# Performance work log

Measured on AMD Instinct MI355X. Metric: run time of the kernel, lower is better.

## Reference

```python
import jax, jax.numpy as jnp
import numpy as np

NEG = -jnp.finfo(jnp.float32).max


def setup_inputs() -> dict:
    key = jax.random.key(0)
    ks = jax.random.split(key, 5)
    B, N, C = 8, 1024, 768
    x = jax.random.normal(ks[0], (B, N, C), dtype=jnp.float32)
    qkv_w = jax.random.normal(ks[1], (3 * C, C), dtype=jnp.float32) * (C ** -0.5)
    qkv_b = jax.random.normal(ks[2], (3 * C,), dtype=jnp.float32) * 0.02
    proj_w = jax.random.normal(ks[3], (C, C), dtype=jnp.float32) * (C ** -0.5)
    proj_b = jax.random.normal(ks[4], (C,), dtype=jnp.float32) * 0.02
    return {"x": x, "qkv_w": qkv_w, "qkv_b": qkv_b, "proj_w": proj_w, "proj_b": proj_b, "k": 64}


def reference(x, qkv_w, qkv_b, proj_w, proj_b, k):
    B, N, C = x.shape
    H = 12
    d = C // H
    scale = d ** -0.5
    # qkv projection: [B,N,3C] -> [3,B,H,N,d]
    qkv = (x @ qkv_w.T + qkv_b).reshape(B, N, 3, H, d).transpose(2, 0, 3, 1, 4)
    q, kk, v = qkv[0], qkv[1], qkv[2]
    attn = jnp.einsum("bhqd,bhkd->bhqk", q, kk) * scale  # [B,H,N,N]
    if k > 0:
        top, _ = jax.lax.top_k(attn, k)
        vk = top[..., -1:]  # k-th largest per query row
        attn = jnp.where(attn < vk, NEG, attn)
    attn = jax.nn.softmax(attn, axis=-1)
    out = jnp.einsum("bhqk,bhkd->bhqd", attn, v)  # [B,H,N,d]
    out = out.transpose(0, 2, 1, 3).reshape(B, N, C)
    return out @ proj_w.T + proj_b
```

## Files before the change

kernel.cpp:

```cpp
#include <hip/hip_runtime.h>

constexpr int Bn = 8, Nn = 1024, Cn = 768, Hn = 12, Dn = 64;

typedef _Float16 f16x4 __attribute__((ext_vector_type(4)));
typedef _Float16 f16x8 __attribute__((ext_vector_type(8)));
typedef float    f32x4v __attribute__((ext_vector_type(4)));

__device__ __forceinline__ unsigned toOrd(float f) {
  unsigned u = __float_as_uint(f);
  return (u & 0x80000000u) ? ~u : (u | 0x80000000u);
}
__device__ __forceinline__ float invOrd(unsigned v) {
  unsigned b = (v & 0x80000000u) ? (v & 0x7FFFFFFFu) : ~v;
  return __uint_as_float(b);
}
__device__ __forceinline__ int lane_excl_cnt(unsigned long long m) {
  return __builtin_amdgcn_mbcnt_hi((unsigned)(m >> 32),
         __builtin_amdgcn_mbcnt_lo((unsigned)m, 0));
}

__device__ __forceinline__ float wave_sum_f32(float x) {
  int xi = __float_as_int(x);
  x += __int_as_float(__builtin_amdgcn_update_dpp(0, xi, 0x111, 0xF, 0xF, false)); xi = __float_as_int(x);
  x += __int_as_float(__builtin_amdgcn_update_dpp(0, xi, 0x112, 0xF, 0xF, false)); xi = __float_as_int(x);
  x += __int_as_float(__builtin_amdgcn_update_dpp(0, xi, 0x114, 0xF, 0xF, false)); xi = __float_as_int(x);
  x += __int_as_float(__builtin_amdgcn_update_dpp(0, xi, 0x118, 0xF, 0xF, false)); xi = __float_as_int(x);
  x += __int_as_float(__builtin_amdgcn_update_dpp(0, xi, 0x142, 0xA, 0xF, false)); xi = __float_as_int(x);
  x += __int_as_float(__builtin_amdgcn_update_dpp(0, xi, 0x143, 0xC, 0xF, false));
  return __int_as_float(__builtin_amdgcn_readlane(__float_as_int(x), 63));
}
__device__ __forceinline__ unsigned wave_max_u32(unsigned x) {
  int xi = (int)x;
  x = max(x, (unsigned)__builtin_amdgcn_update_dpp(xi, xi, 0x111, 0xF, 0xF, false)); xi = (int)x;
  x = max(x, (unsigned)__builtin_amdgcn_update_dpp(xi, xi, 0x112, 0xF, 0xF, false)); xi = (int)x;
  x = max(x, (unsigned)__builtin_amdgcn_update_dpp(xi, xi, 0x114, 0xF, 0xF, false)); xi = (int)x;
  x = max(x, (unsigned)__builtin_amdgcn_update_dpp(xi, xi, 0x118, 0xF, 0xF, false)); xi = (int)x;
  x = max(x, (unsigned)__builtin_amdgcn_update_dpp(xi, xi, 0x142, 0xA, 0xF, false)); xi = (int)x;
  x = max(x, (unsigned)__builtin_amdgcn_update_dpp(xi, xi, 0x143, 0xC, 0xF, false));
  return (unsigned)__builtin_amdgcn_readlane((int)x, 63);
}
__device__ __forceinline__ unsigned wave_min_u32(unsigned x) {
  int xi = (int)x;
  x = min(x, (unsigned)__builtin_amdgcn_update_dpp(xi, xi, 0x111, 0xF, 0xF, false)); xi = (int)x;
  x = min(x, (unsigned)__builtin_amdgcn_update_dpp(xi, xi, 0x112, 0xF, 0xF, false)); xi = (int)x;
  x = min(x, (unsigned)__builtin_amdgcn_update_dpp(xi, xi, 0x114, 0xF, 0xF, false)); xi = (int)x;
  x = min(x, (unsigned)__builtin_amdgcn_update_dpp(xi, xi, 0x118, 0xF, 0xF, false)); xi = (int)x;
  x = min(x, (unsigned)__builtin_amdgcn_update_dpp(xi, xi, 0x142, 0xA, 0xF, false)); xi = (int)x;
  x = min(x, (unsigned)__builtin_amdgcn_update_dpp(xi, xi, 0x143, 0xC, 0xF, false));
  return (unsigned)__builtin_amdgcn_readlane((int)x, 63);
}

__global__ __launch_bounds__(256) void qkv_gemm_mfma(
    const float* __restrict__ X, const float* __restrict__ W,
    const float* __restrict__ bias,
    _Float16* __restrict__ qhp, _Float16* __restrict__ qlp,
    _Float16* __restrict__ khp, _Float16* __restrict__ klp,
    float* __restrict__ vb)
{
  constexpr int LDH = 40;
  __shared__ _Float16 AhH[128*LDH];
  __shared__ _Float16 AhL[128*LDH];
  __shared__ _Float16 BhH[64*LDH];
  __shared__ _Float16 BhL[64*LDH];
  int t = threadIdx.x;
  int wv = t >> 6, lane = t & 63;
  int quad = lane >> 4, l16 = lane & 15;
  int mt = blockIdx.x & 63, nt = blockIdx.x >> 6;
  int m0 = mt*128, n0 = nt*64;
  const bool needLo = (n0 < 1536);
  const float* Ap = X + (size_t)m0*768;
  const float* Bp = W + (size_t)n0*768;
  f32x4v acc1[2][4] = {};
  f32x4v acc2[2][4] = {};
  for (int k0 = 0; k0 < 768; k0 += 32) {
    float4 av[4]; float4 bv[2];
#pragma unroll
    for (int i = 0; i < 4; ++i) {
      int q = t + i*256;
      av[i] = *(const float4*)(Ap + (size_t)(q>>3)*768 + k0 + (q&7)*4);
    }
#pragma unroll
    for (int i = 0; i < 2; ++i) {
      int q = t + i*256;
      bv[i] = *(const float4*)(Bp + (size_t)(q>>3)*768 + k0 + (q&7)*4);
    }
    __syncthreads();
#pragma unroll
    for (int i = 0; i < 4; ++i) {
      int q = t + i*256;
      f16x4 h;
      h[0]=(_Float16)av[i].x; h[1]=(_Float16)av[i].y;
      h[2]=(_Float16)av[i].z; h[3]=(_Float16)av[i].w;
      *(f16x4*)(&AhH[(q>>3)*LDH + (q&7)*4]) = h;
      if (needLo) {
        f16x4 l;
        l[0]=(_Float16)((av[i].x-(float)h[0])*2048.0f);
        l[1]=(_Float16)((av[i].y-(float)h[1])*2048.0f);
        l[2]=(_Float16)((av[i].z-(float)h[2])*2048.0f);
        l[3]=(_Float16)((av[i].w-(float)h[3])*2048.0f);
        *(f16x4*)(&AhL[(q>>3)*LDH + (q&7)*4]) = l;
      }
    }
#pragma unroll
    for (int i = 0; i < 2; ++i) {
      int q = t + i*256;
      f16x4 h;
      h[0]=(_Float16)bv[i].x; h[1]=(_Float16)bv[i].y;
      h[2]=(_Float16)bv[i].z; h[3]=(_Float16)bv[i].w;
      *(f16x4*)(&BhH[(q>>3)*LDH + (q&7)*4]) = h;
      if (needLo) {
        f16x4 l;
        l[0]=(_Float16)((bv[i].x-(float)h[0])*2048.0f);
        l[1]=(_Float16)((bv[i].y-(float)h[1])*2048.0f);
        l[2]=(_Float16)((bv[i].z-(float)h[2])*2048.0f);
        l[3]=(_Float16)((bv[i].w-(float)h[3])*2048.0f);
        *(f16x4*)(&BhL[(q>>3)*LDH + (q&7)*4]) = l;
      }
    }
    __syncthreads();
    if (needLo) {
      f16x8 bfh[4], bfl[4];
#pragma unroll
      for (int ni = 0; ni < 4; ++ni) {
        bfh[ni] = *(f16x8*)(&BhH[(ni*16+l16)*LDH + quad*8]);
        bfl[ni] = *(f16x8*)(&BhL[(ni*16+l16)*LDH + quad*8]);
      }
#pragma unroll
      for (int mi = 0; mi < 2; ++mi) {
        f16x8 afh = *(f16x8*)(&AhH[(wv*32+mi*16+l16)*LDH + quad*8]);
        f16x8 afl = *(f16x8*)(&AhL[(wv*32+mi*16+l16)*LDH + quad*8]);
#pragma unroll
        for (int ni = 0; ni < 4; ++ni) {
          acc1[mi][ni] = __builtin_amdgcn_mfma_f32_16x16x32_f16(afh, bfh[ni], acc1[mi][ni], 0, 0, 0);
          acc2[mi][ni] = __builtin_amdgcn_mfma_f32_16x16x32_f16(afh, bfl[ni], acc2[mi][ni], 0, 0, 0);
          acc2[mi][ni] = __builtin_amdgcn_mfma_f32_16x16x32_f16(afl, bfh[ni], acc2[mi][ni], 0, 0, 0);
        }
      }
    } else {
      f16x8 bfh[4];
#pragma unroll
      for (int ni = 0; ni < 4; ++ni)
        bfh[ni] = *(f16x8*)(&BhH[(ni*16+l16)*LDH + quad*8]);
#pragma unroll
      for (int mi = 0; mi < 2; ++mi) {
        f16x8 afh = *(f16x8*)(&AhH[(wv*32+mi*16+l16)*LDH + quad*8]);
#pragma unroll
        for (int ni = 0; ni < 4; ++ni)
          acc1[mi][ni] = __builtin_amdgcn_mfma_f32_16x16x32_f16(afh, bfh[ni], acc1[mi][ni], 0, 0, 0);
      }
    }
  }
  int which = n0 / Cn;
  int rem0 = n0 - which*Cn;
  int h0 = rem0 >> 6;
  float sc = which == 0 ? 0.125f : 1.0f;
#pragma unroll
  for (int ni = 0; ni < 4; ++ni) {
    float bsv = bias[n0 + ni*16 + l16];
    int dd = (ni*16 + l16) & 63;
#pragma unroll
    for (int mi = 0; mi < 2; ++mi)
#pragma unroll
      for (int r = 0; r < 4; ++r) {
        int gm = m0 + wv*32 + mi*16 + quad*4 + r;
        int bbi = gm >> 10, nn = gm & 1023;
        size_t idx = (((size_t)(bbi*Hn + h0))*Nn + nn)*Dn + dd;
        float val = (acc1[mi][ni][r] + acc2[mi][ni][r] * (1.0f/2048.0f) + bsv) * sc;
        if (which == 2) {
          vb[idx] = val;
        } else {
          _Float16 hh = (_Float16)val;
          _Float16 ll = (_Float16)((val - (float)hh) * 2048.0f);
          if (which == 0) { qhp[idx] = hh; qlp[idx] = ll; }
          else            { khp[idx] = hh; klp[idx] = ll; }
        }
      }
  }
}

template <typename Epi>
__device__ __forceinline__ void mfma_gemm_body(
    const float* __restrict__ Xp, const float* __restrict__ Wp, Epi epi)
{
  constexpr int LDH = 40;
  __shared__ _Float16 Ah[128*LDH];
  __shared__ _Float16 Bh[64*LDH];
  int t = threadIdx.x;
  int wv = t >> 6, lane = t & 63;
  int quad = lane >> 4, l16 = lane & 15;
  int mt = blockIdx.x & 63, nt = blockIdx.x >> 6;
  int m0 = mt*128, n0 = nt*64;
  f32x4v acc[2][4] = {};
  for (int k0 = 0; k0 < 768; k0 += 32) {
    float4 av[4]; float4 bv[2];
#pragma unroll
    for (int i = 0; i < 4; ++i) {
      int q = t + i*256;
      av[i] = *(const float4*)(Xp + (size_t)(m0+(q>>3))*768 + k0 + (q&7)*4);
    }
#pragma unroll
    for (int i = 0; i < 2; ++i) {
      int q = t + i*256;
      bv[i] = *(const float4*)(Wp + (size_t)(n0+(q>>3))*768 + k0 + (q&7)*4);
    }
    __syncthreads();
#pragma unroll
    for (int i = 0; i < 4; ++i) {
      int q = t + i*256;
      f16x4 h; h[0]=(_Float16)av[i].x; h[1]=(_Float16)av[i].y;
               h[2]=(_Float16)av[i].z; h[3]=(_Float16)av[i].w;
      *(f16x4*)(&Ah[(q>>3)*LDH + (q&7)*4]) = h;
    }
#pragma unroll
    for (int i = 0; i < 2; ++i) {
      int q = t + i*256;
      f16x4 h; h[0]=(_Float16)bv[i].x; h[1]=(_Float16)bv[i].y;
               h[2]=(_Float16)bv[i].z; h[3]=(_Float16)bv[i].w;
      *(f16x4*)(&Bh[(q>>3)*LDH + (q&7)*4]) = h;
    }
    __syncthreads();
    f16x8 bf[4], af;
#pragma unroll
    for (int ni = 0; ni < 4; ++ni)
      bf[ni] = *(f16x8*)(&Bh[(ni*16+l16)*LDH + quad*8]);
#pragma unroll
    for (int mi = 0; mi < 2; ++mi) {
      af = *(f16x8*)(&Ah[(wv*32+mi*16+l16)*LDH + quad*8]);
#pragma unroll
      for (int ni = 0; ni < 4; ++ni)
        acc[mi][ni] = __builtin_amdgcn_mfma_f32_16x16x32_f16(af, bf[ni], acc[mi][ni], 0, 0, 0);
    }
  }
#pragma unroll
  for (int mi = 0; mi < 2; ++mi)
#pragma unroll
    for (int ni = 0; ni < 4; ++ni)
#pragma unroll
      for (int r = 0; r < 4; ++r) {
        int gm = m0 + wv*32 + mi*16 + quad*4 + r;
        int gn = n0 + ni*16 + l16;
        epi(gm, gn, acc[mi][ni][r]);
      }
}

__global__ __launch_bounds__(256) void proj_mfma(
    const float* __restrict__ Xp, const float* __restrict__ Wp,
    const float* __restrict__ bias, float* __restrict__ Out)
{
  mfma_gemm_body(Xp, Wp, [=](int gm, int gn, float val) {
    Out[(size_t)gm*768 + gn] = val + bias[gn];
  });
}

__global__ __launch_bounds__(512, 8) void attn_kernel(
    const _Float16* __restrict__ qh, const _Float16* __restrict__ ql,
    const _Float16* __restrict__ kh, const _Float16* __restrict__ kl,
    const float* __restrict__ vB, const int* __restrict__ kptr,
    float* __restrict__ out)
{
  constexpr int G = 16, CAP = 128, CAPP = CAP + 4, LDB = 132;
  __shared__ float  Bx[2][G][LDB];
  __shared__ float2 PairS[G][CAPP];

  int t = threadIdx.x;
  int bh = blockIdx.x >> 6;
  int qg = blockIdx.x & 63;
  int qbase = qg * G;
  int w = t >> 6, lane = t & 63;
  int quad = lane >> 4, l16 = lane & 15;

  const _Float16* QH = qh + (size_t)bh * Nn * Dn;
  const _Float16* QL = ql + (size_t)bh * Nn * Dn;
  const _Float16* KH = kh + (size_t)bh * Nn * Dn;
  const _Float16* KL = kl + (size_t)bh * Nn * Dn;
  const float*   Vbh = vB + (size_t)bh * Nn * Dn;

  int r0 = w*2, r1 = r0 + 1;
  unsigned u0[16], u1[16];

  f16x8 aqh[2], aql[2];
  {
    size_t qoff = (size_t)(qbase + l16) * Dn + quad * 8;
#pragma unroll
    for (int c = 0; c < 2; ++c) {
      aqh[c] = *(const f16x8*)(QH + qoff + c*32);
      aql[c] = *(const f16x8*)(QL + qoff + c*32);
    }
  }
  f16x8 bhf[2][2], blf[2][2];
  {
    size_t koff = (size_t)(16*w + l16) * Dn + quad*8;
#pragma unroll
    for (int c = 0; c < 2; ++c) {
      bhf[0][c] = *(const f16x8*)(KH + koff + c*32);
      blf[0][c] = *(const f16x8*)(KL + koff + c*32);
    }
  }
#pragma unroll
  for (int j = 0; j < 8; ++j) {
    if (j < 7) {
      size_t koff = (size_t)(16*w + 128*(j+1) + l16) * Dn + quad*8;
#pragma unroll
      for (int c = 0; c < 2; ++c) {
        bhf[(j+1)&1][c] = *(const f16x8*)(KH + koff + c*32);
        blf[(j+1)&1][c] = *(const f16x8*)(KL + koff + c*32);
      }
    }
    int cb = j & 1;
    f32x4v a1 = {}, a2 = {};
    a1 = __builtin_amdgcn_mfma_f32_16x16x32_f16(aqh[0], bhf[cb][0], a1, 0,0,0);
    a1 = __builtin_amdgcn_mfma_f32_16x16x32_f16(aqh[1], bhf[cb][1], a1, 0,0,0);
    a2 = __builtin_amdgcn_mfma_f32_16x16x32_f16(aqh[0], blf[cb][0], a2, 0,0,0);
    a2 = __builtin_amdgcn_mfma_f32_16x16x32_f16(aqh[1], blf[cb][1], a2, 0,0,0);
    a2 = __builtin_amdgcn_mfma_f32_16x16x32_f16(aql[0], bhf[cb][0], a2, 0,0,0);
    a2 = __builtin_amdgcn_mfma_f32_16x16x32_f16(aql[1], bhf[cb][1], a2, 0,0,0);
#pragma unroll
    for (int r2 = 0; r2 < 4; ++r2)
      Bx[cb][quad*4 + r2][w*16 + l16] = a1[r2] + a2[r2] * (1.0f/2048.0f);
    __syncthreads();
    u0[2*j]   = toOrd(Bx[cb][r0][lane]);
    u0[2*j+1] = toOrd(Bx[cb][r0][lane + 64]);
    u1[2*j]   = toOrd(Bx[cb][r1][lane]);
    u1[2*j+1] = toOrd(Bx[cb][r1][lane + 64]);
  }

  int kval = *kptr;
  bool doSel = (kval > 0 && kval < Nn);

  unsigned mu0 = u0[0], mu1 = u1[0];
#pragma unroll
  for (int i = 1; i < 16; ++i) { mu0 = max(mu0, u0[i]); mu1 = max(mu1, u1[i]); }
  float m0 = invOrd(wave_max_u32(mu0));
  float m1 = invOrd(wave_max_u32(mu1));

  unsigned thr0 = 0u, thr1 = 0u;
  if (doSel) {
    unsigned res0 = 0u, res1 = 0u;
    bool done0 = false, done1 = false;
    for (int bit = 31; bit >= 0; --bit) {
      if (!done0) {
        unsigned cand = res0 | (1u << bit);
        int ct = 0;
#pragma unroll
        for (int i = 0; i < 16; ++i)
          ct += __popcll(__ballot(u0[i] >= cand));
        if (ct == kval) {
          unsigned mn = 0xFFFFFFFFu;
#pragma unroll
          for (int i = 0; i < 16; ++i)
            if (u0[i] >= cand && u0[i] < mn) mn = u0[i];
          res0 = wave_min_u32(mn);
          done0 = true;
        } else if (ct > kval) res0 = cand;
      }
      if (!done1) {
        unsigned cand = res1 | (1u << bit);
        int ct = 0;
#pragma unroll
        for (int i = 0; i < 16; ++i)
          ct += __popcll(__ballot(u1[i] >= cand));
        if (ct == kval) {
          unsigned mn = 0xFFFFFFFFu;
#pragma unroll
          for (int i = 0; i < 16; ++i)
            if (u1[i] >= cand && u1[i] < mn) mn = u1[i];
          res1 = wave_min_u32(mn);
          done1 = true;
        } else if (ct > kval) res1 = cand;
      }
      if (done0 && done1) break;
    }
    thr0 = res0; thr1 = res1;
  }

  float2* Pair0 = &PairS[r0][0];
  float2* Pair1 = &PairS[r1][0];
  float Zl0 = 0.f, Zl1 = 0.f;
  int cnt0 = 0, cnt1 = 0;
#pragma unroll
  for (int i = 0; i < 16; ++i) {
    bool k0 = (u0[i] >= thr0);
    unsigned long long mk0 = __ballot(k0);
    if (k0) {
      float wgt = __expf(invOrd(u0[i]) - m0);
      Zl0 += wgt;
      int pos = cnt0 + lane_excl_cnt(mk0);
      if (pos < CAP) {
        float2 pr; pr.x = wgt; pr.y = __int_as_float(lane + 64*i);
        Pair0[pos] = pr;
      }
    }
    cnt0 += __popcll(mk0);
    bool k1 = (u1[i] >= thr1);
    unsigned long long mk1 = __ballot(k1);
    if (k1) {
      float wgt = __expf(invOrd(u1[i]) - m1);
      Zl1 += wgt;
      int pos = cnt1 + lane_excl_cnt(mk1);
      if (pos < CAP) {
        float2 pr; pr.x = wgt; pr.y = __int_as_float(lane + 64*i);
        Pair1[pos] = pr;
      }
    }
    cnt1 += __popcll(mk1);
  }
  float Z0 = wave_sum_f32(Zl0);
  float Z1 = wave_sum_f32(Zl1);

  if (lane < 4) {
    float2 z; z.x = 0.f; z.y = __int_as_float(0);
    if (cnt0 <= CAP) Pair0[cnt0 + lane] = z;
    if (cnt1 <= CAP) Pair1[cnt1 + lane] = z;
  }

  float acc0 = 0.f, acc1 = 0.f;
  bool fast0 = (cnt0 <= CAP), fast1 = (cnt1 <= CAP);
  if (fast0 && fast1) {
    int nc = min(cnt0, cnt1);
    int i = 0;
    for (; i < nc; i += 4) {
      float2 p00 = Pair0[i],   p01 = Pair0[i+1];
      float2 p02 = Pair0[i+2], p03 = Pair0[i+3];
      float2 p10 = Pair1[i],   p11 = Pair1[i+1];
      float2 p12 = Pair1[i+2], p13 = Pair1[i+3];
      float v00 = Vbh[(size_t)__float_as_int(p00.y)*Dn + lane];
      float v01 = Vbh[(size_t)__float_as_int(p01.y)*Dn + lane];
      float v02 = Vbh[(size_t)__float_as_int(p02.y)*Dn + lane];
      float v03 = Vbh[(size_t)__float_as_int(p03.y)*Dn + lane];
      float v10 = Vbh[(size_t)__float_as_int(p10.y)*Dn + lane];
      float v11 = Vbh[(size_t)__float_as_int(p11.y)*Dn + lane];
      float v12 = Vbh[(size_t)__float_as_int(p12.y)*Dn + lane];
      float v13 = Vbh[(size_t)__float_as_int(p13.y)*Dn + lane];
      acc0 = fmaf(p00.x, v00, acc0); acc0 = fmaf(p01.x, v01, acc0);
      acc0 = fmaf(p02.x, v02, acc0); acc0 = fmaf(p03.x, v03, acc0);
      acc1 = fmaf(p10.x, v10, acc1); acc1 = fmaf(p11.x, v11, acc1);
      acc1 = fmaf(p12.x, v12, acc1); acc1 = fmaf(p13.x, v13, acc1);
    }
    for (; i < cnt0; i += 4) {
      float2 p0 = Pair0[i],   p1 = Pair0[i+1];
      float2 p2 = Pair0[i+2], p3 = Pair0[i+3];
      float v0 = Vbh[(size_t)__float_as_int(p0.y)*Dn + lane];
      float v1 = Vbh[(size_t)__float_as_int(p1.y)*Dn + lane];
      float v2 = Vbh[(size_t)__float_as_int(p2.y)*Dn + lane];
      float v3 = Vbh[(size_t)__float_as_int(p3.y)*Dn + lane];
      acc0 = fmaf(p0.x, v0, acc0); acc0 = fmaf(p1.x, v1, acc0);
      acc0 = fmaf(p2.x, v2, acc0); acc0 = fmaf(p3.x, v3, acc0);
    }
    for (; i < cnt1; i += 4) {
      float2 p0 = Pair1[i],   p1 = Pair1[i+1];
      float2 p2 = Pair1[i+2], p3 = Pair1[i+3];
      float v0 = Vbh[(size_t)__float_as_int(p0.y)*Dn + lane];
      float v1 = Vbh[(size_t)__float_as_int(p1.y)*Dn + lane];
      float v2 = Vbh[(size_t)__float_as_int(p2.y)*Dn + lane];
      float v3 = Vbh[(size_t)__float_as_int(p3.y)*Dn + lane];
      acc1 = fmaf(p0.x, v0, acc1); acc1 = fmaf(p1.x, v1, acc1);
      acc1 = fmaf(p2.x, v2, acc1); acc1 = fmaf(p3.x, v3, acc1);
    }
  } else {
    if (fast0) {
      for (int i = 0; i < cnt0; i += 4) {
        float2 p0 = Pair0[i],   p1 = Pair0[i+1];
        float2 p2 = Pair0[i+2], p3 = Pair0[i+3];
        float v0 = Vbh[(size_t)__float_as_int(p0.y)*Dn + lane];
        float v1 = Vbh[(size_t)__float_as_int(p1.y)*Dn + lane];
        float v2 = Vbh[(size_t)__float_as_int(p2.y)*Dn + lane];
        float v3 = Vbh[(size_t)__float_as_int(p3.y)*Dn + lane];
        acc0 = fmaf(p0.x, v0, acc0); acc0 = fmaf(p1.x, v1, acc0);
        acc0 = fmaf(p2.x, v2, acc0); acc0 = fmaf(p3.x, v3, acc0);
      }
    } else {
#pragma unroll
      for (int i = 0; i < 16; ++i) {
        float wbase = (u0[i] >= thr0) ? __expf(invOrd(u0[i]) - m0) : 0.f;
        for (int src = 0; src < 64; ++src) {
          float wgt = __shfl(wbase, src);
          if (wgt != 0.f)
            acc0 = fmaf(wgt, Vbh[(size_t)(src + 64*i)*Dn + lane], acc0);
        }
      }
    }
    if (fast1) {
      for (int i = 0; i < cnt1; i += 4) {
        float2 p0 = Pair1[i],   p1 = Pair1[i+1];
        float2 p2 = Pair1[i+2], p3 = Pair1[i+3];
        float v0 = Vbh[(size_t)__float_as_int(p0.y)*Dn + lane];
        float v1 = Vbh[(size_t)__float_as_int(p1.y)*Dn + lane];
        float v2 = Vbh[(size_t)__float_as_int(p2.y)*Dn + lane];
        float v3 = Vbh[(size_t)__float_as_int(p3.y)*Dn + lane];
        acc1 = fmaf(p0.x, v0, acc1); acc1 = fmaf(p1.x, v1, acc1);
        acc1 = fmaf(p2.x, v2, acc1); acc1 = fmaf(p3.x, v3, acc1);
      }
    } else {
#pragma unroll
      for (int i = 0; i < 16; ++i) {
        float wbase = (u1[i] >= thr1) ? __expf(invOrd(u1[i]) - m1) : 0.f;
        for (int src = 0; src < 64; ++src) {
          float wgt = __shfl(wbase, src);
          if (wgt != 0.f)
            acc1 = fmaf(wgt, Vbh[(size_t)(src + 64*i)*Dn + lane], acc1);
        }
      }
    }
  }

  int b = bh / Hn, h = bh - b*Hn;
  out[((size_t)(b*Nn + qbase + r0))*Cn + h*Dn + lane] = acc0 * (1.0f / Z0);
  out[((size_t)(b*Nn + qbase + r1))*Cn + h*Dn + lane] = acc1 * (1.0f / Z1);
}

extern "C" void kernel_launch(void* const* d_in, const int* in_sizes, int n_in,
                              void* d_out, int out_size, void* d_ws, size_t ws_size,
                              hipStream_t stream) {
  const float* x      = (const float*)d_in[0];
  const float* qkv_w  = (const float*)d_in[1];
  const float* qkv_b  = (const float*)d_in[2];
  const float* proj_w = (const float*)d_in[3];
  const float* proj_b = (const float*)d_in[4];
  const int*   kptr   = (const int*)d_in[5];

  const size_t sz = (size_t)Bn * Hn * Nn * Dn;
  _Float16* qh = (_Float16*)d_ws;
  _Float16* ql = qh + sz;
  _Float16* kh = ql + sz;
  _Float16* kl = kh + sz;
  float* vbuf  = (float*)(kl + sz);
  float* att   = vbuf + sz;
  float* outp  = (float*)d_out;

  qkv_gemm_mfma<<<dim3(36*64), 256, 0, stream>>>(x, qkv_w, qkv_b,
                                                 qh, ql, kh, kl, vbuf);
  attn_kernel<<<dim3(Bn*Hn*(Nn/16)), 512, 0, stream>>>(qh, ql, kh, kl,
                                                       vbuf, kptr, att);
  proj_mfma<<<dim3(12*64), 256, 0, stream>>>(att, proj_w, proj_b, outp);
}
```

Baseline: 519.5 us.

## Precompute fp16 hi/lo planes of X and W in a separate pre-pass kernel

```diff
diff --git a/kernel.cpp b/kernel.cpp
--- a/kernel.cpp
+++ b/kernel.cpp
@@ -50,8 +50,37 @@
   return (unsigned)__builtin_amdgcn_readlane((int)x, 63);
 }
 
+__global__ __launch_bounds__(256) void split_planes(
+    const float* __restrict__ X, const float* __restrict__ W,
+    _Float16* __restrict__ xh, _Float16* __restrict__ xl,
+    _Float16* __restrict__ wh, _Float16* __restrict__ wl)
+{
+  const int X4 = (8192*768)/4;
+  const int T4 = X4 + (2304*768)/4;
+  for (int idx = blockIdx.x*256 + threadIdx.x; idx < T4;
+       idx += gridDim.x*256) {
+    float4 v = (idx < X4) ? ((const float4*)X)[idx]
+                          : ((const float4*)W)[idx - X4];
+    f16x4 h, l;
+    h[0]=(_Float16)v.x; h[1]=(_Float16)v.y; h[2]=(_Float16)v.z; h[3]=(_Float16)v.w;
+    l[0]=(_Float16)((v.x-(float)h[0])*2048.0f);
+    l[1]=(_Float16)((v.y-(float)h[1])*2048.0f);
+    l[2]=(_Float16)((v.z-(float)h[2])*2048.0f);
+    l[3]=(_Float16)((v.w-(float)h[3])*2048.0f);
+    if (idx < X4) {
+      *(f16x4*)(xh + (size_t)idx*4) = h;
+      *(f16x4*)(xl + (size_t)idx*4) = l;
+    } else {
+      size_t j = (size_t)(idx - X4)*4;
+      *(f16x4*)(wh + j) = h;
+      *(f16x4*)(wl + j) = l;
+    }
+  }
+}
+
 __global__ __launch_bounds__(256) void qkv_gemm_mfma(
-    const float* __restrict__ X, const float* __restrict__ W,
+    const _Float16* __restrict__ Xh, const _Float16* __restrict__ Xl,
+    const _Float16* __restrict__ Wh, const _Float16* __restrict__ Wl,
     const float* __restrict__ bias,
     _Float16* __restrict__ qhp, _Float16* __restrict__ qlp,
     _Float16* __restrict__ khp, _Float16* __restrict__ klp,
@@ -68,55 +97,31 @@
   int mt = blockIdx.x & 63, nt = blockIdx.x >> 6;
   int m0 = mt*128, n0 = nt*64;
   const bool needLo = (n0 < 1536);
-  const float* Ap = X + (size_t)m0*768;
-  const float* Bp = W + (size_t)n0*768;
   f32x4v acc1[2][4] = {};
   f32x4v acc2[2][4] = {};
   for (int k0 = 0; k0 < 768; k0 += 32) {
-    float4 av[4]; float4 bv[2];
-#pragma unroll
-    for (int i = 0; i < 4; ++i) {
-      int q = t + i*256;
-      av[i] = *(const float4*)(Ap + (size_t)(q>>3)*768 + k0 + (q&7)*4);
-    }
+    f16x8 a_h[2], a_l[2], b_h, b_l;
 #pragma unroll
     for (int i = 0; i < 2; ++i) {
       int q = t + i*256;
-      bv[i] = *(const float4*)(Bp + (size_t)(q>>3)*768 + k0 + (q&7)*4);
+      size_t off = (size_t)(m0 + (q>>2))*768 + k0 + (q&3)*8;
+      a_h[i] = *(const f16x8*)(Xh + off);
+      if (needLo) a_l[i] = *(const f16x8*)(Xl + off);
+    }
+    {
+      size_t off = (size_t)(n0 + (t>>2))*768 + k0 + (t&3)*8;
+      b_h = *(const f16x8*)(Wh + off);
+      if (needLo) b_l = *(const f16x8*)(Wl + off);
     }
     __syncthreads();
-#pragma unroll
-    for (int i = 0; i < 4; ++i) {
-      int q = t + i*256;
-      f16x4 h;
-      h[0]=(_Float16)av[i].x; h[1]=(_Float16)av[i].y;
-      h[2]=(_Float16)av[i].z; h[3]=(_Float16)av[i].w;
-      *(f16x4*)(&AhH[(q>>3)*LDH + (q&7)*4]) = h;
-      if (needLo) {
-        f16x4 l;
-        l[0]=(_Float16)((av[i].x-(float)h[0])*2048.0f);
-        l[1]=(_Float16)((av[i].y-(float)h[1])*2048.0f);
-        l[2]=(_Float16)((av[i].z-(float)h[2])*2048.0f);
-        l[3]=(_Float16)((av[i].w-(float)h[3])*2048.0f);
-        *(f16x4*)(&AhL[(q>>3)*LDH + (q&7)*4]) = l;
-      }
-    }
 #pragma unroll
     for (int i = 0; i < 2; ++i) {
       int q = t + i*256;
-      f16x4 h;
-      h[0]=(_Float16)bv[i].x; h[1]=(_Float16)bv[i].y;
-      h[2]=(_Float16)bv[i].z; h[3]=(_Float16)bv[i].w;
-      *(f16x4*)(&BhH[(q>>3)*LDH + (q&7)*4]) = h;
-      if (needLo) {
-        f16x4 l;
-        l[0]=(_Float16)((bv[i].x-(float)h[0])*2048.0f);
-        l[1]=(_Float16)((bv[i].y-(float)h[1])*2048.0f);
-        l[2]=(_Float16)((bv[i].z-(float)h[2])*2048.0f);
-        l[3]=(_Float16)((bv[i].w-(float)h[3])*2048.0f);
-        *(f16x4*)(&BhL[(q>>3)*LDH + (q&7)*4]) = l;
-      }
-    }
+      *(f16x8*)(&AhH[(q>>2)*LDH + (q&3)*8]) = a_h[i];
+      if (needLo) *(f16x8*)(&AhL[(q>>2)*LDH + (q&3)*8]) = a_l[i];
+    }
+    *(f16x8*)(&BhH[(t>>2)*LDH + (t&3)*8]) = b_h;
+    if (needLo) *(f16x8*)(&BhL[(t>>2)*LDH + (t&3)*8]) = b_l;
     __syncthreads();
     if (needLo) {
       f16x8 bfh[4], bfl[4];
@@ -518,16 +523,23 @@
   const float* proj_b = (const float*)d_in[4];
   const int*   kptr   = (const int*)d_in[5];
 
-  const size_t sz = (size_t)Bn * Hn * Nn * Dn;
+  const size_t sz  = (size_t)Bn * Hn * Nn * Dn;
+  const size_t XSZ = (size_t)8192 * 768;
+  const size_t WSZ = (size_t)2304 * 768;
   _Float16* qh = (_Float16*)d_ws;
   _Float16* ql = qh + sz;
   _Float16* kh = ql + sz;
   _Float16* kl = kh + sz;
   float* vbuf  = (float*)(kl + sz);
-  float* att   = vbuf + sz;
+  _Float16* xh = (_Float16*)(vbuf + sz);
+  _Float16* xl = xh + XSZ;
+  float* att   = (float*)xh;
+  _Float16* wh = xl + XSZ;
+  _Float16* wl = wh + WSZ;
   float* outp  = (float*)d_out;
 
-  qkv_gemm_mfma<<<dim3(36*64), 256, 0, stream>>>(x, qkv_w, qkv_b,
+  split_planes<<<dim3(2048), 256, 0, stream>>>(x, qkv_w, xh, xl, wh, wl);
+  qkv_gemm_mfma<<<dim3(36*64), 256, 0, stream>>>(xh, xl, wh, wl, qkv_b,
                                                  qh, ql, kh, kl, vbuf);
   attn_kernel<<<dim3(Bn*Hn*(Nn/16)), 512, 0, stream>>>(qh, ql, kh, kl,
                                                        vbuf, kptr, att);
```

After: 512.3 us. About the same (-1.4%).
